# Performance work log

Measured on AMD Instinct MI355X. Metric: run time of the kernel, lower is better.

## Reference

```python
import jax, jax.numpy as jnp
import numpy as np


def setup_inputs() -> dict:
    key = jax.random.key(0)
    k1, k2 = jax.random.split(key)
    B, C, N = 32, 512, 4096
    x = jax.random.normal(k1, (B, C, N), dtype=jnp.float32)
    gamma = jax.random.normal(k2, (1,), dtype=jnp.float32)
    return {"x": x, "gamma": gamma}


def reference(x, gamma):
    # x: [B, C, N]. Channel attention: energy = x @ x^T -> [B, C, C]
    energy = jnp.einsum('bcn,bdn->bcd', x, x)
    # inverted score: rowmax - energy, then softmax over last dim
    energy_new = jnp.max(energy, axis=-1, keepdims=True) - energy
    attention = jax.nn.softmax(energy_new, axis=-1)  # [B, C, C]
    out = jnp.einsum('bcd,bdn->bcn', attention, x)
    return gamma * out + x
```

## Files before the change

kernel.cpp:

```cpp
#include <hip/hip_runtime.h>
#include <stdint.h>
#include <stddef.h>

#define NB 32
#define NC 512
#define NN 4096

typedef _Float16 h4_t __attribute__((ext_vector_type(4)));
typedef _Float16 h8_t __attribute__((ext_vector_type(8)));
typedef float    f4_t __attribute__((ext_vector_type(4)));

__device__ __forceinline__ void gload16(const _Float16* g, _Float16* l) {
    __builtin_amdgcn_global_load_lds(
        (const __attribute__((address_space(1))) void*)g,
        (__attribute__((address_space(3))) void*)l, 16, 0, 0);
}


__global__ __launch_bounds__(256) void cast_transpose(
    const float* __restrict__ x, _Float16* __restrict__ Xh,
    _Float16* __restrict__ Xl, _Float16* __restrict__ Xt)
{
    __shared__ __attribute__((aligned(16))) _Float16 tile[64 * 66];
    const int b = blockIdx.z, c0 = blockIdx.y * 64, n0 = blockIdx.x * 64;
    const int t = threadIdx.x;
    const int lr = t >> 4;
    const int lc = (t & 15) * 4;
    const size_t xbase = (size_t)b * NC * NN;

#pragma unroll
    for (int p = 0; p < 4; ++p) {
        const int r = p * 16 + lr;
        const size_t off = xbase + (size_t)(c0 + r) * NN + (n0 + lc);
        const float4 v = *(const float4*)(x + off);
        const _Float16 h0 = (_Float16)v.x, h1 = (_Float16)v.y;
        const _Float16 h2 = (_Float16)v.z, h3 = (_Float16)v.w;
        h4_t hv = {h0, h1, h2, h3};
        *(h4_t*)(Xh + off) = hv;
        h4_t lv = {(_Float16)(v.x - (float)h0), (_Float16)(v.y - (float)h1),
                   (_Float16)(v.z - (float)h2), (_Float16)(v.w - (float)h3)};
        *(h4_t*)(Xl + off) = lv;
        tile[r * 66 + lc + 0] = h0;
        tile[r * 66 + lc + 1] = h1;
        tile[r * 66 + lc + 2] = h2;
        tile[r * 66 + lc + 3] = h3;
    }
    __syncthreads();
    const size_t tbase = (size_t)b * NN * NC;
#pragma unroll
    for (int p = 0; p < 4; ++p) {
        const int rn = p * 16 + lr;
        h4_t w;
        w[0] = tile[(lc + 0) * 66 + rn];
        w[1] = tile[(lc + 1) * 66 + rn];
        w[2] = tile[(lc + 2) * 66 + rn];
        w[3] = tile[(lc + 3) * 66 + rn];
        *(h4_t*)(Xt + tbase + (size_t)(n0 + rn) * NC + (c0 + lc)) = w;
    }
}

__global__ __launch_bounds__(256) void cast_hl(
    const float* __restrict__ x, _Float16* __restrict__ Xh,
    _Float16* __restrict__ Xl)
{
    const size_t total = (size_t)NB * NC * NN / 4;
    for (size_t i = (size_t)blockIdx.x * 256 + threadIdx.x; i < total;
         i += (size_t)gridDim.x * 256) {
        const float4 v = ((const float4*)x)[i];
        const _Float16 h0 = (_Float16)v.x, h1 = (_Float16)v.y;
        const _Float16 h2 = (_Float16)v.z, h3 = (_Float16)v.w;
        h4_t hv = {h0, h1, h2, h3};
        h4_t lv = {(_Float16)(v.x - (float)h0), (_Float16)(v.y - (float)h1),
                   (_Float16)(v.z - (float)h2), (_Float16)(v.w - (float)h3)};
        ((h4_t*)Xh)[i] = hv;
        ((h4_t*)Xl)[i] = lv;
    }
}

__global__ __launch_bounds__(512, 2) void gemm1_energy(
    const _Float16* __restrict__ Xh, const _Float16* __restrict__ Xl,
    float* __restrict__ part, int kch, int nsplit)
{
    __shared__ __attribute__((aligned(16))) _Float16 sAh[2][256 * 32];
    __shared__ __attribute__((aligned(16))) _Float16 sAl[2][256 * 32];
    __shared__ __attribute__((aligned(16))) _Float16 sBh[2][256 * 32];
    __shared__ __attribute__((aligned(16))) _Float16 sBl[2][256 * 32];

    const int flat = blockIdx.x;
    const int cpx  = 12 * nsplit;
    const int swz  = (flat & 7) * cpx + (flat >> 3);
    const int per_b = 3 * nsplit;
    const int b   = swz / per_b;
    const int rem = swz % per_b;
    const int s   = rem / 3;
    const int mem = rem % 3;
    const int ti  = (mem >= 1) ? 1 : 0;
    const int tj  = (mem == 2) ? 1 : 0;
    const bool diag = (mem != 1);

    const int t = threadIdx.x;
    const int wave = t >> 6, lane = t & 63;
    const int wr = wave >> 2, wc = wave & 3;
    const int fr = lane & 15, fq = lane >> 4;
    const int hi4 = fq * 4;

    const int rr  = t >> 2;
    const int sck = (((t & 3) ^ ((t >> 3) & 3)) * 8);

    const size_t xb = (size_t)b * NC * NN + (size_t)s * kch;
    const _Float16* gAh = Xh + xb + (size_t)(ti * 256 + rr) * NN + sck;
    const _Float16* gAl = Xl + xb + (size_t)(ti * 256 + rr) * NN + sck;
    const _Float16* gBh = Xh + xb + (size_t)(tj * 256 + rr) * NN + sck;
    const _Float16* gBl = Xl + xb + (size_t)(tj * 256 + rr) * NN + sck;
    const size_t P = (size_t)128 * NN;

    f4_t acc[4][8];
#pragma unroll
    for (int nf = 0; nf < 4; ++nf)
#pragma unroll
        for (int m = 0; m < 8; ++m) acc[nf][m] = (f4_t){0.f, 0.f, 0.f, 0.f};

#define STG1(buf, k0)                                                        \
    {                                                                        \
        gload16(gAh + (k0),     &sAh[buf][0] + t * 8);                       \
        gload16(gAh + (k0) + P, &sAh[buf][0] + 4096 + t * 8);                \
        gload16(gAl + (k0),     &sAl[buf][0] + t * 8);                       \
        gload16(gAl + (k0) + P, &sAl[buf][0] + 4096 + t * 8);                \
        if (!diag) {                                                         \
            gload16(gBh + (k0),     &sBh[buf][0] + t * 8);                   \
            gload16(gBh + (k0) + P, &sBh[buf][0] + 4096 + t * 8);            \
            gload16(gBl + (k0),     &sBl[buf][0] + t * 8);                   \
            gload16(gBl + (k0) + P, &sBl[buf][0] + 4096 + t * 8);            \
        }                                                                    \
    }

    STG1(0, 0);
    __syncthreads();

    const int nIter = kch >> 5;
    for (int it = 0; it < nIter; ++it) {
        const int cur = it & 1;
        if (it + 1 < nIter) STG1(cur ^ 1, (it + 1) * 32);

        const _Float16* cAh = &sAh[cur][0];
        const _Float16* cAl = &sAl[cur][0];
        const _Float16* cBh = diag ? cAh : &sBh[cur][0];
        const _Float16* cBl = diag ? cAl : &sBl[cur][0];

        h8_t bh_[4], bl_[4];
#pragma unroll
        for (int nf = 0; nf < 4; ++nf) {
            const int br = wc * 64 + nf * 16 + fr;
            const int so = (fq ^ ((br >> 1) & 3)) * 8;
            bh_[nf] = *(const h8_t*)(cBh + br * 32 + so);
            bl_[nf] = *(const h8_t*)(cBl + br * 32 + so);
        }
#pragma unroll
        for (int m = 0; m < 8; ++m) {
            const int ar = wr * 128 + m * 16 + fr;
            const int so = (fq ^ ((ar >> 1) & 3)) * 8;
            const h8_t ah = *(const h8_t*)(cAh + ar * 32 + so);
            const h8_t al = *(const h8_t*)(cAl + ar * 32 + so);
#pragma unroll
            for (int nf = 0; nf < 4; ++nf) {
                acc[nf][m] = __builtin_amdgcn_mfma_f32_16x16x32_f16(bh_[nf], ah, acc[nf][m], 0, 0, 0);
                acc[nf][m] = __builtin_amdgcn_mfma_f32_16x16x32_f16(bl_[nf], ah, acc[nf][m], 0, 0, 0);
                acc[nf][m] = __builtin_amdgcn_mfma_f32_16x16x32_f16(bh_[nf], al, acc[nf][m], 0, 0, 0);
            }
        }
        __syncthreads();
    }
#undef STG1

    float* pb = part + ((size_t)s * NB + b) * (NC * NC);
#pragma unroll
    for (int m = 0; m < 8; ++m) {
        const int i = ti * 256 + wr * 128 + m * 16 + fr;
#pragma unroll
        for (int nf = 0; nf < 4; ++nf) {
            const int jjb = tj * 256 + wc * 64 + nf * 16 + hi4;
            *(f4_t*)(pb + (size_t)i * NC + jjb) = acc[nf][m];
            if (!diag) {
#pragma unroll
                for (int j = 0; j < 4; ++j)
                    pb[(size_t)(jjb + j) * NC + i] = acc[nf][m][j];
            }
        }
    }
}

__global__ __launch_bounds__(256) void softmax_inv(
    const float* __restrict__ part, _Float16* __restrict__ attn, int nsplit)
{
    const int row = blockIdx.x * 4 + (threadIdx.x >> 6);
    const int lane = threadIdx.x & 63;
    const size_t roff = (size_t)row * NC;

    float4 a0 = {0.f, 0.f, 0.f, 0.f}, a1 = {0.f, 0.f, 0.f, 0.f};
    for (int s = 0; s < nsplit; ++s) {
        const float4* p = (const float4*)(part + (size_t)s * NB * NC * NC + roff);
        const float4 v0 = p[lane], v1 = p[64 + lane];
        a0.x += v0.x; a0.y += v0.y; a0.z += v0.z; a0.w += v0.w;
        a1.x += v1.x; a1.y += v1.y; a1.z += v1.z; a1.w += v1.w;
    }

    float mn = fminf(fminf(fminf(a0.x, a0.y), fminf(a0.z, a0.w)),
                     fminf(fminf(a1.x, a1.y), fminf(a1.z, a1.w)));
#pragma unroll
    for (int off = 32; off; off >>= 1) mn = fminf(mn, __shfl_xor(mn, off));

    const float w0 = __expf(mn - a0.x), w1 = __expf(mn - a0.y);
    const float w2 = __expf(mn - a0.z), w3 = __expf(mn - a0.w);
    const float w4 = __expf(mn - a1.x), w5 = __expf(mn - a1.y);
    const float w6 = __expf(mn - a1.z), w7 = __expf(mn - a1.w);
    float sum = ((w0 + w1) + (w2 + w3)) + ((w4 + w5) + (w6 + w7));
#pragma unroll
    for (int off = 32; off; off >>= 1) sum += __shfl_xor(sum, off);
    const float inv = 1.0f / sum;

    h4_t o0 = {(_Float16)(w0 * inv), (_Float16)(w1 * inv),
               (_Float16)(w2 * inv), (_Float16)(w3 * inv)};
    h4_t o1 = {(_Float16)(w4 * inv), (_Float16)(w5 * inv),
               (_Float16)(w6 * inv), (_Float16)(w7 * inv)};
    ((h4_t*)(attn + roff))[lane] = o0;
    ((h4_t*)(attn + roff))[64 + lane] = o1;
}

__global__ __launch_bounds__(256) void transpose_h(
    const _Float16* __restrict__ Xh, _Float16* __restrict__ Xt)
{
    __shared__ __attribute__((aligned(16))) _Float16 tile[64 * 66];
    const int b = blockIdx.z, c0 = blockIdx.y * 64, n0 = blockIdx.x * 64;
    const int t = threadIdx.x;
    const int lr = t >> 4;
    const int lc = (t & 15) * 4;
    const size_t hbase = (size_t)b * NC * NN;

#pragma unroll
    for (int p = 0; p < 4; ++p) {
        const int r = p * 16 + lr;
        const h4_t v = *(const h4_t*)(Xh + hbase + (size_t)(c0 + r) * NN + (n0 + lc));
        tile[r * 66 + lc + 0] = v[0];
        tile[r * 66 + lc + 1] = v[1];
        tile[r * 66 + lc + 2] = v[2];
        tile[r * 66 + lc + 3] = v[3];
    }
    __syncthreads();
    const size_t tbase = (size_t)b * NN * NC;
#pragma unroll
    for (int p = 0; p < 4; ++p) {
        const int rn = p * 16 + lr;
        h4_t w;
        w[0] = tile[(lc + 0) * 66 + rn];
        w[1] = tile[(lc + 1) * 66 + rn];
        w[2] = tile[(lc + 2) * 66 + rn];
        w[3] = tile[(lc + 3) * 66 + rn];
        *(h4_t*)(Xt + tbase + (size_t)(n0 + rn) * NC + (c0 + lc)) = w;
    }
}

__global__ __launch_bounds__(512, 2) void gemm2_out(
    const _Float16* __restrict__ attn, const _Float16* __restrict__ Xt,
    const _Float16* __restrict__ Xh, const float* __restrict__ gammap,
    float* __restrict__ out)
{
    __shared__ __attribute__((aligned(16))) _Float16 sA[4][256 * 32];
    __shared__ __attribute__((aligned(16))) _Float16 sB[4][256 * 32];

    const int flat = blockIdx.x;
    const int swz  = (flat & 7) * 128 + (flat >> 3);
    const int b    = swz >> 5;
    const int memb = swz & 31;
    const int brow = (memb & 1) * 256;
    const int bcol = (memb >> 1) * 256;

    const int t = threadIdx.x;
    const int wave = t >> 6, lane = t & 63;
    const int wr = wave >> 2, wc = wave & 3;
    const int fr = lane & 15, fq = lane >> 4;
    const int hi4 = fq * 4;

    const int rr  = t >> 2;
    const int sck = (((t & 3) ^ ((t >> 3) & 3)) * 8);
    const _Float16* gA = attn + (size_t)b * NC * NC + (size_t)(brow + rr) * NC + sck;
    const _Float16* gB = Xt   + (size_t)b * NN * NC + (size_t)(bcol + rr) * NC + sck;
    const size_t P = (size_t)128 * NC;

    f4_t acc[4][8];
#pragma unroll
    for (int nf = 0; nf < 4; ++nf)
#pragma unroll
        for (int m = 0; m < 8; ++m) acc[nf][m] = (f4_t){0.f, 0.f, 0.f, 0.f};

#define STG2(buf, k0)                                                        \
    {                                                                        \
        gload16(gA + (k0),     &sA[buf][0] + t * 8);                         \
        gload16(gA + (k0) + P, &sA[buf][0] + 4096 + t * 8);                  \
        gload16(gB + (k0),     &sB[buf][0] + t * 8);                         \
        gload16(gB + (k0) + P, &sB[buf][0] + 4096 + t * 8);                  \
    }

    STG2(0, 0);
    STG2(1, 32);
    STG2(2, 64);

#pragma unroll
    for (int it = 0; it < 16; ++it) {
        if (it <= 13)       asm volatile("s_waitcnt vmcnt(8)" ::: "memory");
        else if (it == 14)  asm volatile("s_waitcnt vmcnt(4)" ::: "memory");
        else                asm volatile("s_waitcnt vmcnt(0)" ::: "memory");
        __builtin_amdgcn_s_barrier();
        if (it <= 12) STG2((it + 3) & 3, (it + 3) * 32);

        const _Float16* cA = &sA[it & 3][0];
        const _Float16* cB = &sB[it & 3][0];
        h8_t b_[4];
#pragma unroll
        for (int nf = 0; nf < 4; ++nf) {
            const int br = wc * 64 + nf * 16 + fr;
            b_[nf] = *(const h8_t*)(cB + br * 32 + ((fq ^ ((br >> 1) & 3)) * 8));
        }
#pragma unroll
        for (int m = 0; m < 8; ++m) {
            const int ar = wr * 128 + m * 16 + fr;
            const h8_t a = *(const h8_t*)(cA + ar * 32 + ((fq ^ ((ar >> 1) & 3)) * 8));
#pragma unroll
            for (int nf = 0; nf < 4; ++nf)
                acc[nf][m] = __builtin_amdgcn_mfma_f32_16x16x32_f16(
                    b_[nf], a, acc[nf][m], 0, 0, 0);
        }
    }
#undef STG2

    const float g = gammap[0];
    const _Float16* xb = Xh + (size_t)b * NC * NN;
    float* ob = out + (size_t)b * NC * NN;
#pragma unroll
    for (int m = 0; m < 8; ++m) {
        const int c_ = brow + wr * 128 + m * 16 + fr;
#pragma unroll
        for (int nf = 0; nf < 4; ++nf) {
            const int n_ = bcol + wc * 64 + nf * 16 + hi4;
            const size_t off = (size_t)c_ * NN + n_;
            const h4_t xv = *(const h4_t*)(xb + off);
            f4_t o;
#pragma unroll
            for (int j = 0; j < 4; ++j)
                o[j] = g * acc[nf][m][j] + (float)xv[j];
            *(f4_t*)(ob + off) = o;
        }
    }
}

extern "C" void kernel_launch(void* const* d_in, const int* in_sizes, int n_in,
                              void* d_out, int out_size, void* d_ws, size_t ws_size,
                              hipStream_t stream)
{
    const float* x     = (const float*)d_in[0];
    const float* gamma = (const float*)d_in[1];
    float* out = (float*)d_out;
    char* ws = (char*)d_ws;

    if (ws_size >= 553648128ull) {
        _Float16* Xh   = (_Float16*)(ws);
        _Float16* Xl   = (_Float16*)(ws + 134217728ull);
        _Float16* Xt   = (_Float16*)(ws + 268435456ull);
        _Float16* attn = (_Float16*)(ws + 402653184ull);
        float*    part = (float*)   (ws + 419430400ull);
        const int nsplit = (ws_size >= 687865856ull) ? 8 : 4;
        const int kch = NN / nsplit;

        cast_transpose<<<dim3(NN / 64, NC / 64, NB), 256, 0, stream>>>(x, Xh, Xl, Xt);
        gemm1_energy<<<dim3(3 * nsplit * NB), 512, 0, stream>>>(Xh, Xl, part, kch, nsplit);
        softmax_inv<<<dim3(NB * NC / 4), 256, 0, stream>>>(part, attn, nsplit);
        gemm2_out<<<dim3(1024), 512, 0, stream>>>(attn, Xt, Xh, gamma, out);
    } else {
        _Float16* Xh   = (_Float16*)(ws);
        _Float16* XlXt = (_Float16*)(ws + 134217728ull);
        _Float16* attn = (_Float16*)(ws + 268435456ull);
        float*    part = (float*)   (ws + 285212672ull);

        cast_hl<<<dim3(2048), 256, 0, stream>>>(x, Xh, XlXt);
        gemm1_energy<<<dim3(3 * 4 * NB), 512, 0, stream>>>(Xh, XlXt, part, NN / 4, 4);
        softmax_inv<<<dim3(NB * NC / 4), 256, 0, stream>>>(part, attn, 4);
        transpose_h<<<dim3(NN / 64, NC / 64, NB), 256, 0, stream>>>(Xh, XlXt);
        gemm2_out<<<dim3(1024), 512, 0, stream>>>(attn, XlXt, Xh, gamma, out);
    }
}
```

Before: 492.1 us.

## Enlarge gemm2 tile to full 512 rows with triple-buffered pipeline

The second GEMM now has each block compute all 512 channel rows for a 256-column strip, using 8x8 MFMA fragments per wave. This halves the grid and stops the attention matrix from being reloaded by two row blocks. The LDS pipeline moves from a 4-stage to a 3-stage rotating buffer with split-half compute, s_setprio around the MFMA bursts, and extra barriers. The block-to-XCD mapping also changes so each batch stays on one XCD. In exchange, occupancy drops to one block per CU, with a doubled accumulator register footprint and possible spills.

```diff
diff --git a/kernel.cpp b/kernel.cpp
--- a/kernel.cpp
+++ b/kernel.cpp
@@ -15,6 +15,9 @@
         (const __attribute__((address_space(1))) void*)g,
         (__attribute__((address_space(3))) void*)l, 16, 0, 0);
 }
+
+#define BARF() { asm volatile("" ::: "memory"); __builtin_amdgcn_s_barrier(); \
+                 asm volatile("" ::: "memory"); }
 
 
 __global__ __launch_bounds__(256) void cast_transpose(
@@ -259,88 +262,108 @@
     }
 }
 
-__global__ __launch_bounds__(512, 2) void gemm2_out(
+__global__ __launch_bounds__(512, 1) void gemm2_out(
     const _Float16* __restrict__ attn, const _Float16* __restrict__ Xt,
     const _Float16* __restrict__ Xh, const float* __restrict__ gammap,
     float* __restrict__ out)
 {
-    __shared__ __attribute__((aligned(16))) _Float16 sA[4][256 * 32];
-    __shared__ __attribute__((aligned(16))) _Float16 sB[4][256 * 32];
+    __shared__ __attribute__((aligned(16))) _Float16 sA[3][512 * 32];
+    __shared__ __attribute__((aligned(16))) _Float16 sB[3][256 * 32];
 
     const int flat = blockIdx.x;
-    const int swz  = (flat & 7) * 128 + (flat >> 3);
-    const int b    = swz >> 5;
-    const int memb = swz & 31;
-    const int brow = (memb & 1) * 256;
-    const int bcol = (memb >> 1) * 256;
+    const int xcd  = flat & 7;
+    const int slot = flat >> 3;
+    const int b    = xcd + 8 * (slot >> 4);
+    const int nt   = slot & 15;
 
     const int t = threadIdx.x;
     const int wave = t >> 6, lane = t & 63;
-    const int wr = wave >> 2, wc = wave & 3;
+    const int wrow = wave & 3, wcol = wave >> 2;
     const int fr = lane & 15, fq = lane >> 4;
     const int hi4 = fq * 4;
 
     const int rr  = t >> 2;
     const int sck = (((t & 3) ^ ((t >> 3) & 3)) * 8);
-    const _Float16* gA = attn + (size_t)b * NC * NC + (size_t)(brow + rr) * NC + sck;
-    const _Float16* gB = Xt   + (size_t)b * NN * NC + (size_t)(bcol + rr) * NC + sck;
-    const size_t P = (size_t)128 * NC;
-
-    f4_t acc[4][8];
-#pragma unroll
-    for (int nf = 0; nf < 4; ++nf)
+    const _Float16* gA = attn + (size_t)b * NC * NC + (size_t)rr * NC + sck;
+    const _Float16* gB = Xt + (size_t)b * NN * NC +
+                         (size_t)(nt * 256 + rr) * NC + sck;
+
+    f4_t acc[8][8];
+#pragma unroll
+    for (int nf = 0; nf < 8; ++nf)
 #pragma unroll
         for (int m = 0; m < 8; ++m) acc[nf][m] = (f4_t){0.f, 0.f, 0.f, 0.f};
 
-#define STG2(buf, k0)                                                        \
+#define STG2(i, k0)                                                          \
     {                                                                        \
-        gload16(gA + (k0),     &sA[buf][0] + t * 8);                         \
-        gload16(gA + (k0) + P, &sA[buf][0] + 4096 + t * 8);                  \
-        gload16(gB + (k0),     &sB[buf][0] + t * 8);                         \
-        gload16(gB + (k0) + P, &sB[buf][0] + 4096 + t * 8);                  \
+        gload16(gA + (k0),                    &sA[i][0] + t * 8);            \
+        gload16(gA + (k0) + (size_t)128 * NC, &sA[i][0] + 4096 + t * 8);     \
+        gload16(gA + (k0) + (size_t)256 * NC, &sA[i][0] + 8192 + t * 8);     \
+        gload16(gA + (k0) + (size_t)384 * NC, &sA[i][0] + 12288 + t * 8);    \
+        gload16(gB + (k0),                    &sB[i][0] + t * 8);            \
+        gload16(gB + (k0) + (size_t)128 * NC, &sB[i][0] + 4096 + t * 8);     \
+    }
+
+#define CMP2(i)                                                              \
+    {                                                                        \
+        const _Float16* cA = &sA[i][0];                                      \
+        const _Float16* cB = &sB[i][0];                                      \
+        h8_t b_[8];                                                          \
+        _Pragma("unroll")                                                    \
+        for (int nf = 0; nf < 8; ++nf) {                                     \
+            const int br = wcol * 128 + nf * 16 + fr;                        \
+            b_[nf] = *(const h8_t*)(cB + br * 32 + ((fq ^ ((br >> 1) & 3)) * 8)); \
+        }                                                                    \
+        _Pragma("unroll")                                                    \
+        for (int half = 0; half < 2; ++half) {                               \
+            h8_t a_[4];                                                      \
+            _Pragma("unroll")                                                \
+            for (int mm = 0; mm < 4; ++mm) {                                 \
+                const int ar = wrow * 128 + (half * 4 + mm) * 16 + fr;       \
+                a_[mm] = *(const h8_t*)(cA + ar * 32 + ((fq ^ ((ar >> 1) & 3)) * 8)); \
+            }                                                                \
+            __builtin_amdgcn_s_setprio(1);                                   \
+            _Pragma("unroll")                                                \
+            for (int mm = 0; mm < 4; ++mm)                                   \
+                _Pragma("unroll")                                            \
+                for (int nf = 0; nf < 8; ++nf)                               \
+                    acc[nf][half * 4 + mm] = __builtin_amdgcn_mfma_f32_16x16x32_f16( \
+                        b_[nf], a_[mm], acc[nf][half * 4 + mm], 0, 0, 0);    \
+            __builtin_amdgcn_s_setprio(0);                                   \
+            BARF();                                                          \
+        }                                                                    \
     }
 
     STG2(0, 0);
     STG2(1, 32);
-    STG2(2, 64);
-
-#pragma unroll
-    for (int it = 0; it < 16; ++it) {
-        if (it <= 13)       asm volatile("s_waitcnt vmcnt(8)" ::: "memory");
-        else if (it == 14)  asm volatile("s_waitcnt vmcnt(4)" ::: "memory");
-        else                asm volatile("s_waitcnt vmcnt(0)" ::: "memory");
-        __builtin_amdgcn_s_barrier();
-        if (it <= 12) STG2((it + 3) & 3, (it + 3) * 32);
-
-        const _Float16* cA = &sA[it & 3][0];
-        const _Float16* cB = &sB[it & 3][0];
-        h8_t b_[4];
-#pragma unroll
-        for (int nf = 0; nf < 4; ++nf) {
-            const int br = wc * 64 + nf * 16 + fr;
-            b_[nf] = *(const h8_t*)(cB + br * 32 + ((fq ^ ((br >> 1) & 3)) * 8));
-        }
-#pragma unroll
-        for (int m = 0; m < 8; ++m) {
-            const int ar = wr * 128 + m * 16 + fr;
-            const h8_t a = *(const h8_t*)(cA + ar * 32 + ((fq ^ ((ar >> 1) & 3)) * 8));
-#pragma unroll
-            for (int nf = 0; nf < 4; ++nf)
-                acc[nf][m] = __builtin_amdgcn_mfma_f32_16x16x32_f16(
-                    b_[nf], a, acc[nf][m], 0, 0, 0);
-        }
-    }
+
+    int i0 = 0, i1 = 1, i2 = 2;
+    for (int it = 0; it < 14; ++it) {
+        STG2(i2, (it + 2) * 32);
+        asm volatile("s_waitcnt vmcnt(12)" ::: "memory");
+        BARF();
+        CMP2(i0);
+        const int tmp = i0; i0 = i1; i1 = i2; i2 = tmp;
+    }
+    asm volatile("s_waitcnt vmcnt(6)" ::: "memory");
+    BARF();
+    CMP2(i0);
+    { const int tmp = i0; i0 = i1; i1 = i2; i2 = tmp; }
+    asm volatile("s_waitcnt vmcnt(0)" ::: "memory");
+    BARF();
+    CMP2(i0);
 #undef STG2
+#undef CMP2
 
     const float g = gammap[0];
     const _Float16* xb = Xh + (size_t)b * NC * NN;
     float* ob = out + (size_t)b * NC * NN;
 #pragma unroll
     for (int m = 0; m < 8; ++m) {
-        const int c_ = brow + wr * 128 + m * 16 + fr;
-#pragma unroll
-        for (int nf = 0; nf < 4; ++nf) {
-            const int n_ = bcol + wc * 64 + nf * 16 + hi4;
+        const int c_ = wrow * 128 + m * 16 + fr;
+#pragma unroll
+        for (int nf = 0; nf < 8; ++nf) {
+            const int n_ = nt * 256 + wcol * 128 + nf * 16 + hi4;
             const size_t off = (size_t)c_ * NN + n_;
             const h4_t xv = *(const h4_t*)(xb + off);
             f4_t o;
@@ -373,7 +396,7 @@
         cast_transpose<<<dim3(NN / 64, NC / 64, NB), 256, 0, stream>>>(x, Xh, Xl, Xt);
         gemm1_energy<<<dim3(3 * nsplit * NB), 512, 0, stream>>>(Xh, Xl, part, kch, nsplit);
         softmax_inv<<<dim3(NB * NC / 4), 256, 0, stream>>>(part, attn, nsplit);
-        gemm2_out<<<dim3(1024), 512, 0, stream>>>(attn, Xt, Xh, gamma, out);
+        gemm2_out<<<dim3(512), 512, 0, stream>>>(attn, Xt, Xh, gamma, out);
     } else {
         _Float16* Xh   = (_Float16*)(ws);
         _Float16* XlXt = (_Float16*)(ws + 134217728ull);
@@ -384,6 +407,6 @@
         gemm1_energy<<<dim3(3 * 4 * NB), 512, 0, stream>>>(Xh, XlXt, part, NN / 4, 4);
         softmax_inv<<<dim3(NB * NC / 4), 256, 0, stream>>>(part, attn, 4);
         transpose_h<<<dim3(NN / 64, NC / 64, NB), 256, 0, stream>>>(Xh, XlXt);
-        gemm2_out<<<dim3(1024), 512, 0, stream>>>(attn, XlXt, Xh, gamma, out);
-    }
-}
+        gemm2_out<<<dim3(512), 512, 0, stream>>>(attn, XlXt, Xh, gamma, out);
+    }
+}
```

After: 875.0 us. 1.78x slower.
